# Kernel tuning notes

Hardware: AMD Instinct MI355X
Metric: run time of the kernel (lower is better)

Reference implementation:

```python
import jax, jax.numpy as jnp
import numpy as np

LAYERS, STACKS = 10, 4
DILATIONS = [2 ** l for _ in range(STACKS) for l in range(LAYERS)]  # 40 blocks


def setup_inputs() -> dict:
    key = jax.random.key(0)
    ks = jax.random.split(key, 7)
    B, C, L, SC, NB = 4, 64, 8192, 256, len(DILATIONS)
    scale = 0.05  # keep 40 stacked residual blocks numerically tame
    return {
        "x": jax.random.normal(ks[0], (B, C, L), dtype=jnp.float32),
        "dc_w": jax.random.normal(ks[1], (NB, C, C, 2), dtype=jnp.float32) * scale,
        "dc_b": jax.random.normal(ks[2], (NB, C), dtype=jnp.float32) * scale,
        "conv_w": jax.random.normal(ks[3], (NB, C, C), dtype=jnp.float32) * scale,
        "conv_b": jax.random.normal(ks[4], (NB, C), dtype=jnp.float32) * scale,
        "skip_w": jax.random.normal(ks[5], (NB, SC, C), dtype=jnp.float32) * scale,
        "skip_b": jax.random.normal(ks[6], (NB, SC), dtype=jnp.float32) * scale,
        "skip_size": 4096,
    }


def reference(x, dc_w, dc_b, conv_w, conv_b, skip_w, skip_b, skip_size):
    # x: [B, res_ch, L]; returns stacked skips [n_blocks, B, skip_ch, skip_size]
    out = x
    skips = []
    for i, d in enumerate(DILATIONS):
        h = (jnp.einsum('oi,bil->bol', dc_w[i, :, :, 0], out[:, :, :-d])
             + jnp.einsum('oi,bil->bol', dc_w[i, :, :, 1], out[:, :, d:])
             + dc_b[i][None, :, None])
        g = jax.nn.relu(h)
        r = jnp.einsum('oi,bil->bol', conv_w[i], g) + conv_b[i][None, :, None]
        out = r + out[:, :, -r.shape[2]:]  # residual on aligned (last) timesteps
        s = jnp.einsum('oi,bil->bol', skip_w[i], g) + skip_b[i][None, :, None]
        skips.append(s[:, :, -skip_size:])
    return jnp.stack(skips)
```

## Files before the change

### kernel.cpp

```cpp
#include <hip/hip_runtime.h>


#define CC    64
#define SCC   256
#define BB    4
#define LL0   8192
#define NBLK  40
#define SKIPN 4096

typedef __attribute__((ext_vector_type(8))) short bf16x8;
typedef __attribute__((ext_vector_type(4))) float f32x4;
typedef unsigned short us;

__device__ __forceinline__ us f2bf(float f) {
    union { float f; unsigned u; } v; v.f = f;
    return (us)((v.u + 0x7FFF + ((v.u >> 16) & 1)) >> 16);
}
__device__ __forceinline__ unsigned pk2(float a, float b) {
    return (unsigned)f2bf(a) | ((unsigned)f2bf(b) << 16);
}
__device__ __forceinline__ uint2 pk4(f32x4 v) {
    return (uint2){pk2(v[0], v[1]), pk2(v[2], v[3])};
}
__device__ __forceinline__ bf16x8 pack8(f32x4 u0, f32x4 u1) {
    bf16x8 r;
    r[0]=(short)f2bf(u0[0]); r[1]=(short)f2bf(u0[1]);
    r[2]=(short)f2bf(u0[2]); r[3]=(short)f2bf(u0[3]);
    r[4]=(short)f2bf(u1[0]); r[5]=(short)f2bf(u1[1]);
    r[6]=(short)f2bf(u1[2]); r[7]=(short)f2bf(u1[3]);
    return r;
}
__device__ __forceinline__ int sws(int r, int c) {
    return (r << 6) + ((((c >> 3) ^ r) & 7) << 3) + (c & 7);
}
__device__ __forceinline__ int scb(int s, int chunk) {
    return (s << 6) + (((chunk ^ (s & 7)) & 7) << 3);
}

__global__ __launch_bounds__(256) void prep_kernel(
    const float* __restrict__ x, float* __restrict__ xt_out,
    const float* __restrict__ dc_w, const float* __restrict__ conv_w,
    const float* __restrict__ skip_w,
    us* __restrict__ wcat, us* __restrict__ cwb, us* __restrict__ swb)
{
    if (blockIdx.x < 512) {
        __shared__ float tile[64][65];
        const int b = blockIdx.x >> 7, t0 = (blockIdx.x & 127) * 64;
        const int tid = threadIdx.x;
        #pragma unroll
        for (int p = 0; p < 4; ++p) {
            const int c = p * 16 + (tid >> 4), j = tid & 15;
            const float4 v = *(const float4*)(x + ((size_t)b * CC + c) * LL0 + t0 + j * 4);
            tile[c][j*4+0]=v.x; tile[c][j*4+1]=v.y; tile[c][j*4+2]=v.z; tile[c][j*4+3]=v.w;
        }
        __syncthreads();
        #pragma unroll
        for (int p = 0; p < 4; ++p) {
            const int r = p * 16 + (tid >> 4), h = tid & 15;
            float4 v = {tile[h*4+0][r], tile[h*4+1][r], tile[h*4+2][r], tile[h*4+3][r]};
            *(float4*)(xt_out + ((size_t)b * LL0 + t0 + r) * CC + h * 4) = v;
        }
        return;
    }
    const int n_sw = NBLK * SCC * CC, n_cw = NBLK * CC * CC, n_wc = NBLK * CC * 128;
    for (int idx = (blockIdx.x - 512) * blockDim.x + threadIdx.x; idx < n_sw;
         idx += 1024 * blockDim.x) {
        swb[idx] = f2bf(skip_w[idx]);
        if (idx < n_cw) cwb[idx] = f2bf(conv_w[idx]);
        if (idx < n_wc) {
            const int i = idx >> 13, o = (idx >> 7) & 63, kk = idx & 127;
            wcat[idx] = f2bf(dc_w[(((i * CC + o) * CC) + (kk & 63)) * 2 + (kk >> 6)]);
        }
    }
}

template<int NW>
__device__ __forceinline__ void skip_body(
    int e, int blk0,
    const us* __restrict__ g_all, const us* __restrict__ swb,
    const float* __restrict__ skip_b, float* __restrict__ out)
{
    constexpr int ROWS = NW * 16;
    constexpr int TPB = (SKIPN / ROWS) * BB;
    const int tid = threadIdx.x, lane = tid & 63, wv = tid >> 6;
    const int j = blk0 + e / TPB;
    const int id = e % TPB;
    const int tt = id % (SKIPN / ROWS);
    const int b  = id / (SKIPN / ROWS);
    const us* g  = g_all + ((size_t)j * BB + b) * SKIPN * CC;
    const us* sw = swb + (size_t)j * SCC * CC;
    const float* sb = skip_b + j * SCC;
    float* op = out + ((size_t)j * BB + b) * SCC * SKIPN;

    const int trow = tt * ROWS + wv * 16 + (lane & 15);
    bf16x8 a[2];
    a[0] = *(const bf16x8*)(g + (size_t)trow * CC + (lane >> 4) * 8);
    a[1] = *(const bf16x8*)(g + (size_t)trow * CC + 32 + (lane >> 4) * 8);
    const int tstore = tt * ROWS + wv * 16 + ((lane >> 4) << 2);
    #pragma unroll 4
    for (int n = 0; n < 16; ++n) {
        const int sc = n * 16 + (lane & 15);
        const float bias = sb[sc];
        f32x4 acc = (f32x4){bias, bias, bias, bias};
        const us* wrow = sw + sc * CC + (lane >> 4) * 8;
        acc = __builtin_amdgcn_mfma_f32_16x16x32_bf16(a[0], *(const bf16x8*)(wrow), acc, 0, 0, 0);
        acc = __builtin_amdgcn_mfma_f32_16x16x32_bf16(a[1], *(const bf16x8*)(wrow + 32), acc, 0, 0, 0);
        *(float4*)(op + (size_t)sc * SKIPN + tstore) = (float4){acc[0], acc[1], acc[2], acc[3]};
    }
}

__global__ __launch_bounds__(512) void fused6_kernel(
    const float* __restrict__ cur, float* __restrict__ nxt,
    const us* __restrict__ wcat_all, const us* __restrict__ cwb_all,
    const float* __restrict__ db_all, const float* __restrict__ cb_all,
    us* __restrict__ g_all, int blk0, int Lin, int ntiles,
    const us* __restrict__ swb, const float* __restrict__ skip_b,
    float* __restrict__ out, int pb0)
{
    const int wg = blockIdx.x, chain = BB * ntiles;
    if (wg >= chain) { skip_body<8>(wg - chain, pb0, g_all, swb, skip_b, out); return; }

    constexpr int TOUT = 96, R0 = 159, RCAP = 160;
    __shared__ __align__(16) float sm[RCAP * CC];
    __shared__ __align__(16) us  scr[8 * 16 * CC];

    const int tid = threadIdx.x, lane = tid & 63, wv = tid >> 6;
    const int b = wg / ntiles, t0 = (wg % ntiles) * TOUT;
    const float* src = cur + (size_t)b * LL0 * CC;
    const int s = lane & 15, q = lane >> 4;
    us* myscr = scr + wv * (16 * CC);

    for (int base = 0; base < R0; base += 32) {
        const int row = base + (tid >> 4);
        const int h4 = (tid & 15) * 4;
        if (row < R0) {
            int gt = t0 + row; if (gt > Lin - 1) gt = Lin - 1;
            *(f32x4*)(sm + sws(row, h4)) = *(const f32x4*)(src + (size_t)gt * CC + h4);
        }
    }
    __syncthreads();

    int Rcur = R0, Lj = Lin;
    for (int j = 0; j < 6; ++j) {
        const int d = 1 << j;
        const int Rn = Rcur - d;
        Lj -= d;
        const us* wj = wcat_all + (size_t)(blk0 + j) * CC * 128;
        const us* cj = cwb_all + (size_t)(blk0 + j) * CC * CC;
        const float* dbj = db_all + (blk0 + j) * CC;
        const float* cbj = cb_all + (blk0 + j) * CC;
        const int wbase = Lj - SKIPN;
        us* gdst = g_all + ((size_t)(blk0 + j) * BB + b) * SKIPN * CC;

        f32x4 r2[2][4];
        #pragma unroll
        for (int fi = 0; fi < 2; ++fi) {
            const int fg = wv + fi * 8;
            const bool act = fg * 16 < Rn;
            if (act) {
                const int t = fg * 16 + s;
                const int tc = t > Rn - 1 ? Rn - 1 : t;
                bf16x8 af0 = pack8(*(const f32x4*)(sm + sws(tc, q * 8)),
                                   *(const f32x4*)(sm + sws(tc, q * 8 + 4)));
                bf16x8 af1 = pack8(*(const f32x4*)(sm + sws(tc, 32 + q * 8)),
                                   *(const f32x4*)(sm + sws(tc, 36 + q * 8)));
                bf16x8 af2 = pack8(*(const f32x4*)(sm + sws(tc + d, q * 8)),
                                   *(const f32x4*)(sm + sws(tc + d, q * 8 + 4)));
                bf16x8 af3 = pack8(*(const f32x4*)(sm + sws(tc + d, 32 + q * 8)),
                                   *(const f32x4*)(sm + sws(tc + d, 36 + q * 8)));
                #pragma unroll
                for (int n = 0; n < 4; ++n) {
                    const int o0 = n * 16 + q * 4;
                    f32x4 acc = *(const f32x4*)(dbj + o0);
                    const us* wr = wj + (n * 16 + s) * 128 + q * 8;
                    acc = __builtin_amdgcn_mfma_f32_16x16x32_bf16(*(const bf16x8*)(wr),      af0, acc, 0, 0, 0);
                    acc = __builtin_amdgcn_mfma_f32_16x16x32_bf16(*(const bf16x8*)(wr + 32), af1, acc, 0, 0, 0);
                    acc = __builtin_amdgcn_mfma_f32_16x16x32_bf16(*(const bf16x8*)(wr + 64), af2, acc, 0, 0, 0);
                    acc = __builtin_amdgcn_mfma_f32_16x16x32_bf16(*(const bf16x8*)(wr + 96), af3, acc, 0, 0, 0);
                    #pragma unroll
                    for (int r = 0; r < 4; ++r) acc[r] = acc[r] > 0.f ? acc[r] : 0.f;
                    *(uint2*)(myscr + scb(s, n * 2 + (q >> 1)) + (q & 1) * 4) = pk4(acc);
                }
                {
                    const int gt = t0 + t;
                    if (t < Rn && gt >= wbase && gt < Lj) {
                        us* gr = gdst + (size_t)(gt - wbase) * CC;
                        #pragma unroll
                        for (int h = 0; h < 2; ++h) {
                            const int ck = q * 2 + h;
                            *(bf16x8*)(gr + ck * 8) = *(const bf16x8*)(myscr + scb(s, ck));
                        }
                    }
                }
                bf16x8 g0 = *(const bf16x8*)(myscr + scb(s, q));
                bf16x8 g1 = *(const bf16x8*)(myscr + scb(s, 4 + q));
                #pragma unroll
                for (int n = 0; n < 4; ++n) {
                    const int o0 = n * 16 + q * 4;
                    f32x4 r = *(const f32x4*)(cbj + o0);
                    const us* wr = cj + (n * 16 + s) * CC + q * 8;
                    r = __builtin_amdgcn_mfma_f32_16x16x32_bf16(*(const bf16x8*)(wr),      g0, r, 0, 0, 0);
                    r = __builtin_amdgcn_mfma_f32_16x16x32_bf16(*(const bf16x8*)(wr + 32), g1, r, 0, 0, 0);
                    r += *(const f32x4*)(sm + sws(tc + d, o0));
                    r2[fi][n] = r;
                }
            }
        }
        __syncthreads();
        #pragma unroll
        for (int fi = 0; fi < 2; ++fi) {
            const int fg = wv + fi * 8;
            const int t = fg * 16 + s;
            if (t < Rn) {
                #pragma unroll
                for (int n = 0; n < 4; ++n)
                    *(f32x4*)(sm + sws(t, n * 16 + q * 4)) = r2[fi][n];
            }
        }
        __syncthreads();
        Rcur = Rn;
    }

    float* dst = nxt + (size_t)b * LL0 * CC;
    for (int base = 0; base < TOUT; base += 32) {
        const int row = base + (tid >> 4);
        const int h4 = (tid & 15) * 4;
        const int gt = t0 + row;
        if (row < TOUT && gt < Lj)
            *(float4*)(dst + (size_t)gt * CC + h4) = *(const float4*)(sm + sws(row, h4));
    }
}

template<int D>
__global__ __launch_bounds__(256) void pair_kernel(
    const float* __restrict__ cur, float* __restrict__ nxt,
    const us* __restrict__ wA, const us* __restrict__ wB,
    const us* __restrict__ cA, const us* __restrict__ cB,
    const float* __restrict__ dbA, const float* __restrict__ dbB,
    const float* __restrict__ cbA, const float* __restrict__ cbB,
    us* __restrict__ gA_out, us* __restrict__ gB_out,
    int Lin, int ntB,
    const us* __restrict__ g_all, const us* __restrict__ swb,
    const float* __restrict__ skip_b, float* __restrict__ out, int pb0)
{
    const int wg = blockIdx.x, chain = BB * ntB;
    if (wg >= chain) { skip_body<4>(wg - chain, pb0, g_all, swb, skip_b, out); return; }

    __shared__ __align__(16) float xs[4 * 32 * CC];
    __shared__ __align__(16) float ms[2 * 32 * CC];
    __shared__ __align__(16) us  scr[4 * 16 * CC];

    const int tid = threadIdx.x, lane = tid & 63, wv = tid >> 6;
    const int b = wg / ntB, T0 = (wg % ntB) * 32;
    const float* src = cur + (size_t)b * LL0 * CC;
    const int s = lane & 15, q = lane >> 4;
    us* myscr = scr + wv * (16 * CC);
    const int LoutA = Lin - D, Lout2 = Lin - 3 * D;

    #pragma unroll
    for (int p = 0; p < 8; ++p) {
        const int row = p * 16 + (tid >> 4);
        const int st = row >> 5, r = row & 31;
        const int h4 = (tid & 15) * 4;
        int gt = T0 + st * D + r; if (gt > Lin - 1) gt = Lin - 1;
        *(f32x4*)(xs + st * (32 * CC) + sws(r, h4)) =
            *(const f32x4*)(src + (size_t)gt * CC + h4);
    }
    __syncthreads();

    {
        const int m = wv >> 1, rA = (wv & 1) * 16 + s;
        const int tA = T0 + m * 2 * D + rA;
        const float* x0 = xs + (2 * m) * (32 * CC);
        const float* x1 = xs + (2 * m + 1) * (32 * CC);
        bf16x8 af0 = pack8(*(const f32x4*)(x0 + sws(rA, q * 8)),
                           *(const f32x4*)(x0 + sws(rA, q * 8 + 4)));
        bf16x8 af1 = pack8(*(const f32x4*)(x0 + sws(rA, 32 + q * 8)),
                           *(const f32x4*)(x0 + sws(rA, 36 + q * 8)));
        bf16x8 af2 = pack8(*(const f32x4*)(x1 + sws(rA, q * 8)),
                           *(const f32x4*)(x1 + sws(rA, q * 8 + 4)));
        bf16x8 af3 = pack8(*(const f32x4*)(x1 + sws(rA, 32 + q * 8)),
                           *(const f32x4*)(x1 + sws(rA, 36 + q * 8)));
        #pragma unroll
        for (int n = 0; n < 4; ++n) {
            const int o0 = n * 16 + q * 4;
            f32x4 acc = *(const f32x4*)(dbA + o0);
            const us* wr = wA + (n * 16 + s) * 128 + q * 8;
            acc = __builtin_amdgcn_mfma_f32_16x16x32_bf16(*(const bf16x8*)(wr),      af0, acc, 0, 0, 0);
            acc = __builtin_amdgcn_mfma_f32_16x16x32_bf16(*(const bf16x8*)(wr + 32), af1, acc, 0, 0, 0);
            acc = __builtin_amdgcn_mfma_f32_16x16x32_bf16(*(const bf16x8*)(wr + 64), af2, acc, 0, 0, 0);
            acc = __builtin_amdgcn_mfma_f32_16x16x32_bf16(*(const bf16x8*)(wr + 96), af3, acc, 0, 0, 0);
            #pragma unroll
            for (int r = 0; r < 4; ++r) acc[r] = acc[r] > 0.f ? acc[r] : 0.f;
            *(uint2*)(myscr + scb(s, n * 2 + (q >> 1)) + (q & 1) * 4) = pk4(acc);
        }
        {
            const int wbA = LoutA - SKIPN;
            const bool own = (m == 0) || (tA >= ntB * 32);
            if (own && tA >= wbA && tA < LoutA) {
                us* gr = gA_out + ((size_t)b * SKIPN + (tA - wbA)) * CC;
                #pragma unroll
                for (int h = 0; h < 2; ++h) {
                    const int ck = q * 2 + h;
                    *(bf16x8*)(gr + ck * 8) = *(const bf16x8*)(myscr + scb(s, ck));
                }
            }
        }
        bf16x8 g0 = *(const bf16x8*)(myscr + scb(s, q));
        bf16x8 g1 = *(const bf16x8*)(myscr + scb(s, 4 + q));
        #pragma unroll
        for (int n = 0; n < 4; ++n) {
            const int o0 = n * 16 + q * 4;
            f32x4 r = *(const f32x4*)(cbA + o0);
            const us* wr = cA + (n * 16 + s) * CC + q * 8;
            r = __builtin_amdgcn_mfma_f32_16x16x32_bf16(*(const bf16x8*)(wr),      g0, r, 0, 0, 0);
            r = __builtin_amdgcn_mfma_f32_16x16x32_bf16(*(const bf16x8*)(wr + 32), g1, r, 0, 0, 0);
            r += *(const f32x4*)(x1 + sws(rA, o0));
            *(f32x4*)(ms + m * (32 * CC) + sws(rA, o0)) = r;
        }
    }
    __syncthreads();

    {
        const int rB = (wv & 1) * 16 + s;
        const int tB = T0 + rB;
        const bool lead = wv < 2;
        const float* m0 = ms;
        const float* m1 = ms + 32 * CC;
        bf16x8 af0 = pack8(*(const f32x4*)(m0 + sws(rB, q * 8)),
                           *(const f32x4*)(m0 + sws(rB, q * 8 + 4)));
        bf16x8 af1 = pack8(*(const f32x4*)(m0 + sws(rB, 32 + q * 8)),
                           *(const f32x4*)(m0 + sws(rB, 36 + q * 8)));
        bf16x8 af2 = pack8(*(const f32x4*)(m1 + sws(rB, q * 8)),
                           *(const f32x4*)(m1 + sws(rB, q * 8 + 4)));
        bf16x8 af3 = pack8(*(const f32x4*)(m1 + sws(rB, 32 + q * 8)),
                           *(const f32x4*)(m1 + sws(rB, 36 + q * 8)));
        #pragma unroll
        for (int n = 0; n < 4; ++n) {
            const int o0 = n * 16 + q * 4;
            f32x4 acc = *(const f32x4*)(dbB + o0);
            const us* wr = wB + (n * 16 + s) * 128 + q * 8;
            acc = __builtin_amdgcn_mfma_f32_16x16x32_bf16(*(const bf16x8*)(wr),      af0, acc, 0, 0, 0);
            acc = __builtin_amdgcn_mfma_f32_16x16x32_bf16(*(const bf16x8*)(wr + 32), af1, acc, 0, 0, 0);
            acc = __builtin_amdgcn_mfma_f32_16x16x32_bf16(*(const bf16x8*)(wr + 64), af2, acc, 0, 0, 0);
            acc = __builtin_amdgcn_mfma_f32_16x16x32_bf16(*(const bf16x8*)(wr + 96), af3, acc, 0, 0, 0);
            #pragma unroll
            for (int r = 0; r < 4; ++r) acc[r] = acc[r] > 0.f ? acc[r] : 0.f;
            *(uint2*)(myscr + scb(s, n * 2 + (q >> 1)) + (q & 1) * 4) = pk4(acc);
        }
        {
            const int wbB = Lout2 - SKIPN;
            if (lead && tB >= wbB && tB < Lout2) {
                us* gr = gB_out + ((size_t)b * SKIPN + (tB - wbB)) * CC;
                #pragma unroll
                for (int h = 0; h < 2; ++h) {
                    const int ck = q * 2 + h;
                    *(bf16x8*)(gr + ck * 8) = *(const bf16x8*)(myscr + scb(s, ck));
                }
            }
        }
        bf16x8 g0 = *(const bf16x8*)(myscr + scb(s, q));
        bf16x8 g1 = *(const bf16x8*)(myscr + scb(s, 4 + q));
        float* dst = nxt + (size_t)b * LL0 * CC;
        #pragma unroll
        for (int n = 0; n < 4; ++n) {
            const int o0 = n * 16 + q * 4;
            f32x4 r = *(const f32x4*)(cbB + o0);
            const us* wr = cB + (n * 16 + s) * CC + q * 8;
            r = __builtin_amdgcn_mfma_f32_16x16x32_bf16(*(const bf16x8*)(wr),      g0, r, 0, 0, 0);
            r = __builtin_amdgcn_mfma_f32_16x16x32_bf16(*(const bf16x8*)(wr + 32), g1, r, 0, 0, 0);
            r += *(const f32x4*)(m1 + sws(rB, o0));
            if (lead && tB < Lout2)
                *(f32x4*)(dst + (size_t)tB * CC + o0) = r;
        }
    }
}

__global__ __launch_bounds__(256) void skip_kernel(
    const us* __restrict__ g_all, const us* __restrict__ swb,
    const float* __restrict__ skip_b, float* __restrict__ out, int blk0)
{
    skip_body<4>(blockIdx.x, blk0, g_all, swb, skip_b, out);
}

extern "C" void kernel_launch(void* const* d_in, const int* in_sizes, int n_in,
                              void* d_out, int out_size, void* d_ws, size_t ws_size,
                              hipStream_t stream)
{
    const float* x      = (const float*)d_in[0];
    const float* dc_w   = (const float*)d_in[1];
    const float* dc_b   = (const float*)d_in[2];
    const float* conv_w = (const float*)d_in[3];
    const float* conv_b = (const float*)d_in[4];
    const float* skip_w = (const float*)d_in[5];
    const float* skip_b = (const float*)d_in[6];
    float* out = (float*)d_out;

    char* ws = (char*)d_ws;
    float* bufA = (float*)ws;  ws += (size_t)BB * LL0 * CC * 4;
    float* bufB = (float*)ws;  ws += (size_t)BB * LL0 * CC * 4;
    us* g_all = (us*)ws;       ws += (size_t)NBLK * BB * SKIPN * CC * 2;
    us* wcat  = (us*)ws;       ws += (size_t)NBLK * CC * 128 * 2;
    us* cwb   = (us*)ws;       ws += (size_t)NBLK * CC * CC * 2;
    us* swb   = (us*)ws;       ws += (size_t)NBLK * SCC * CC * 2;

    prep_kernel<<<1536, 256, 0, stream>>>(x, bufA, dc_w, conv_w, skip_w, wcat, cwb, swb);

    float* bufs[2] = {bufA, bufB};
    const size_t GSZ = (size_t)BB * SKIPN * CC;
    int Lc = LL0, blk = 0, q = 0, produced = 0, skipped = 0;
    for (int st = 0; st < 4; ++st) {
        {
            const int Lout = Lc - 63;
            const int nt = (Lout + 95) / 96;
            int cap = produced - skipped; if (cap > 4) cap = 4;
            fused6_kernel<<<dim3(BB * nt + cap * 128), 512, 0, stream>>>(
                bufs[q & 1], bufs[(q + 1) & 1], wcat, cwb, dc_b, conv_b,
                g_all, blk, Lc, nt, swb, skip_b, out, skipped);
            skipped += cap; produced += 6; blk += 6; Lc = Lout; ++q;
        }
        #pragma unroll
        for (int pi = 0; pi < 2; ++pi) {
            const int D = pi == 0 ? 64 : 256;
            const int Lout2 = Lc - 3 * D;
            const int nt = (Lout2 + 31) / 32;
            int cap = produced - skipped; if (cap > 4) cap = 4;
            const int grid = BB * nt + cap * 256;
            if (D == 64)
                pair_kernel<64><<<dim3(grid), 256, 0, stream>>>(
                    bufs[q & 1], bufs[(q + 1) & 1],
                    wcat + (size_t)blk * CC * 128, wcat + (size_t)(blk + 1) * CC * 128,
                    cwb + (size_t)blk * CC * CC, cwb + (size_t)(blk + 1) * CC * CC,
                    dc_b + blk * CC, dc_b + (blk + 1) * CC,
                    conv_b + blk * CC, conv_b + (blk + 1) * CC,
                    g_all + (size_t)blk * GSZ, g_all + (size_t)(blk + 1) * GSZ,
                    Lc, nt, g_all, swb, skip_b, out, skipped);
            else
                pair_kernel<256><<<dim3(grid), 256, 0, stream>>>(
                    bufs[q & 1], bufs[(q + 1) & 1],
                    wcat + (size_t)blk * CC * 128, wcat + (size_t)(blk + 1) * CC * 128,
                    cwb + (size_t)blk * CC * CC, cwb + (size_t)(blk + 1) * CC * CC,
                    dc_b + blk * CC, dc_b + (blk + 1) * CC,
                    conv_b + blk * CC, conv_b + (blk + 1) * CC,
                    g_all + (size_t)blk * GSZ, g_all + (size_t)(blk + 1) * GSZ,
                    Lc, nt, g_all, swb, skip_b, out, skipped);
            skipped += cap; produced += 2; blk += 2; Lc = Lout2; ++q;
        }
    }
    const int rem = NBLK - skipped;
    if (rem > 0)
        skip_kernel<<<dim3(rem * 256), 256, 0, stream>>>(g_all, swb, skip_b, out, skipped);
}
```

Baseline: 770.5 us.

## Fuse skip projection into residual chain kernels and keep bf16 activation copies in LDS

```diff
diff --git a/kernel.cpp b/kernel.cpp
--- a/kernel.cpp
+++ b/kernel.cpp
@@ -22,15 +22,10 @@
 __device__ __forceinline__ uint2 pk4(f32x4 v) {
     return (uint2){pk2(v[0], v[1]), pk2(v[2], v[3])};
 }
-__device__ __forceinline__ bf16x8 pack8(f32x4 u0, f32x4 u1) {
-    bf16x8 r;
-    r[0]=(short)f2bf(u0[0]); r[1]=(short)f2bf(u0[1]);
-    r[2]=(short)f2bf(u0[2]); r[3]=(short)f2bf(u0[3]);
-    r[4]=(short)f2bf(u1[0]); r[5]=(short)f2bf(u1[1]);
-    r[6]=(short)f2bf(u1[2]); r[7]=(short)f2bf(u1[3]);
-    return r;
-}
 __device__ __forceinline__ int sws(int r, int c) {
+    return (r << 6) + ((((c >> 3) ^ r) & 7) << 3) + (c & 7);
+}
+__device__ __forceinline__ int swh(int r, int c) {
     return (r << 6) + ((((c >> 3) ^ r) & 7) << 3) + (c & 7);
 }
 __device__ __forceinline__ int scb(int s, int chunk) {
@@ -74,38 +69,32 @@
     }
 }
 
-template<int NW>
-__device__ __forceinline__ void skip_body(
-    int e, int blk0,
-    const us* __restrict__ g_all, const us* __restrict__ swb,
-    const float* __restrict__ skip_b, float* __restrict__ out)
-{
-    constexpr int ROWS = NW * 16;
-    constexpr int TPB = (SKIPN / ROWS) * BB;
-    const int tid = threadIdx.x, lane = tid & 63, wv = tid >> 6;
-    const int j = blk0 + e / TPB;
-    const int id = e % TPB;
-    const int tt = id % (SKIPN / ROWS);
-    const int b  = id / (SKIPN / ROWS);
-    const us* g  = g_all + ((size_t)j * BB + b) * SKIPN * CC;
-    const us* sw = swb + (size_t)j * SCC * CC;
-    const float* sb = skip_b + j * SCC;
-    float* op = out + ((size_t)j * BB + b) * SCC * SKIPN;
-
-    const int trow = tt * ROWS + wv * 16 + (lane & 15);
-    bf16x8 a[2];
-    a[0] = *(const bf16x8*)(g + (size_t)trow * CC + (lane >> 4) * 8);
-    a[1] = *(const bf16x8*)(g + (size_t)trow * CC + 32 + (lane >> 4) * 8);
-    const int tstore = tt * ROWS + wv * 16 + ((lane >> 4) << 2);
+__device__ __forceinline__ void skip16(
+    bf16x8 g0, bf16x8 g1,
+    const us* __restrict__ sw, const float* __restrict__ sb,
+    float* __restrict__ op, int tbase, int wb, int Lend,
+    int s, int q, int nlo, int nhi)
+{
+    if (tbase + 15 < wb || tbase >= Lend) return;
+    const int t4 = tbase + q * 4;
+    const bool fullvec = (t4 >= wb) && (t4 + 3 < Lend);
     #pragma unroll 4
-    for (int n = 0; n < 16; ++n) {
-        const int sc = n * 16 + (lane & 15);
+    for (int n = nlo; n < nhi; ++n) {
+        const int sc = n * 16 + s;
         const float bias = sb[sc];
         f32x4 acc = (f32x4){bias, bias, bias, bias};
-        const us* wrow = sw + sc * CC + (lane >> 4) * 8;
-        acc = __builtin_amdgcn_mfma_f32_16x16x32_bf16(a[0], *(const bf16x8*)(wrow), acc, 0, 0, 0);
-        acc = __builtin_amdgcn_mfma_f32_16x16x32_bf16(a[1], *(const bf16x8*)(wrow + 32), acc, 0, 0, 0);
-        *(float4*)(op + (size_t)sc * SKIPN + tstore) = (float4){acc[0], acc[1], acc[2], acc[3]};
+        const us* wr = sw + sc * CC + q * 8;
+        acc = __builtin_amdgcn_mfma_f32_16x16x32_bf16(g0, *(const bf16x8*)(wr),      acc, 0, 0, 0);
+        acc = __builtin_amdgcn_mfma_f32_16x16x32_bf16(g1, *(const bf16x8*)(wr + 32), acc, 0, 0, 0);
+        if (fullvec) {
+            *(float4*)(op + (size_t)sc * SKIPN + (t4 - wb)) =
+                (float4){acc[0], acc[1], acc[2], acc[3]};
+        } else {
+            #pragma unroll
+            for (int r = 0; r < 4; ++r)
+                if (t4 + r >= wb && t4 + r < Lend)
+                    op[(size_t)sc * SKIPN + (t4 + r - wb)] = acc[r];
+        }
     }
 }
 
@@ -113,19 +102,18 @@
     const float* __restrict__ cur, float* __restrict__ nxt,
     const us* __restrict__ wcat_all, const us* __restrict__ cwb_all,
     const float* __restrict__ db_all, const float* __restrict__ cb_all,
-    us* __restrict__ g_all, int blk0, int Lin, int ntiles,
-    const us* __restrict__ swb, const float* __restrict__ skip_b,
-    float* __restrict__ out, int pb0)
-{
-    const int wg = blockIdx.x, chain = BB * ntiles;
-    if (wg >= chain) { skip_body<8>(wg - chain, pb0, g_all, swb, skip_b, out); return; }
-
+    const us* __restrict__ swb_all, const float* __restrict__ sb_all,
+    float* __restrict__ out_all, int blk0, int Lin, int ntiles)
+{
     constexpr int TOUT = 96, R0 = 159, RCAP = 160;
     __shared__ __align__(16) float sm[RCAP * CC];
+    __shared__ __align__(16) us  smb[RCAP * CC];
     __shared__ __align__(16) us  scr[8 * 16 * CC];
 
     const int tid = threadIdx.x, lane = tid & 63, wv = tid >> 6;
-    const int b = wg / ntiles, t0 = (wg % ntiles) * TOUT;
+    const int b = blockIdx.x / ntiles, tix = blockIdx.x % ntiles;
+    const int t0 = tix * TOUT;
+    const bool lastt = (tix == ntiles - 1);
     const float* src = cur + (size_t)b * LL0 * CC;
     const int s = lane & 15, q = lane >> 4;
     us* myscr = scr + wv * (16 * CC);
@@ -135,7 +123,9 @@
         const int h4 = (tid & 15) * 4;
         if (row < R0) {
             int gt = t0 + row; if (gt > Lin - 1) gt = Lin - 1;
-            *(f32x4*)(sm + sws(row, h4)) = *(const f32x4*)(src + (size_t)gt * CC + h4);
+            f32x4 v = *(const f32x4*)(src + (size_t)gt * CC + h4);
+            *(f32x4*)(sm + sws(row, h4)) = v;
+            *(uint2*)(smb + swh(row, h4)) = pk4(v);
         }
     }
     __syncthreads();
@@ -147,27 +137,23 @@
         Lj -= d;
         const us* wj = wcat_all + (size_t)(blk0 + j) * CC * 128;
         const us* cj = cwb_all + (size_t)(blk0 + j) * CC * CC;
+        const us* sj = swb_all + (size_t)(blk0 + j) * SCC * CC;
         const float* dbj = db_all + (blk0 + j) * CC;
         const float* cbj = cb_all + (blk0 + j) * CC;
-        const int wbase = Lj - SKIPN;
-        us* gdst = g_all + ((size_t)(blk0 + j) * BB + b) * SKIPN * CC;
+        const float* sbj = sb_all + (blk0 + j) * SCC;
+        float* opj = out_all + ((size_t)(blk0 + j) * BB + b) * SCC * SKIPN;
 
         f32x4 r2[2][4];
         #pragma unroll
         for (int fi = 0; fi < 2; ++fi) {
             const int fg = wv + fi * 8;
-            const bool act = fg * 16 < Rn;
-            if (act) {
+            if (fg * 16 < Rn) {
                 const int t = fg * 16 + s;
                 const int tc = t > Rn - 1 ? Rn - 1 : t;
-                bf16x8 af0 = pack8(*(const f32x4*)(sm + sws(tc, q * 8)),
-                                   *(const f32x4*)(sm + sws(tc, q * 8 + 4)));
-                bf16x8 af1 = pack8(*(const f32x4*)(sm + sws(tc, 32 + q * 8)),
-                                   *(const f32x4*)(sm + sws(tc, 36 + q * 8)));
-                bf16x8 af2 = pack8(*(const f32x4*)(sm + sws(tc + d, q * 8)),
-                                   *(const f32x4*)(sm + sws(tc + d, q * 8 + 4)));
-                bf16x8 af3 = pack8(*(const f32x4*)(sm + sws(tc + d, 32 + q * 8)),
-                                   *(const f32x4*)(sm + sws(tc + d, 36 + q * 8)));
+                bf16x8 af0 = *(const bf16x8*)(smb + swh(tc,     q * 8));
+                bf16x8 af1 = *(const bf16x8*)(smb + swh(tc,     32 + q * 8));
+                bf16x8 af2 = *(const bf16x8*)(smb + swh(tc + d, q * 8));
+                bf16x8 af3 = *(const bf16x8*)(smb + swh(tc + d, 32 + q * 8));
                 #pragma unroll
                 for (int n = 0; n < 4; ++n) {
                     const int o0 = n * 16 + q * 4;
@@ -181,17 +167,6 @@
                     for (int r = 0; r < 4; ++r) acc[r] = acc[r] > 0.f ? acc[r] : 0.f;
                     *(uint2*)(myscr + scb(s, n * 2 + (q >> 1)) + (q & 1) * 4) = pk4(acc);
                 }
-                {
-                    const int gt = t0 + t;
-                    if (t < Rn && gt >= wbase && gt < Lj) {
-                        us* gr = gdst + (size_t)(gt - wbase) * CC;
-                        #pragma unroll
-                        for (int h = 0; h < 2; ++h) {
-                            const int ck = q * 2 + h;
-                            *(bf16x8*)(gr + ck * 8) = *(const bf16x8*)(myscr + scb(s, ck));
-                        }
-                    }
-                }
                 bf16x8 g0 = *(const bf16x8*)(myscr + scb(s, q));
                 bf16x8 g1 = *(const bf16x8*)(myscr + scb(s, 4 + q));
                 #pragma unroll
@@ -204,6 +179,10 @@
                     r += *(const f32x4*)(sm + sws(tc + d, o0));
                     r2[fi][n] = r;
                 }
+                const bool own96 = (fi == 0 && wv < 6);
+                if (own96 || lastt)
+                    skip16(g0, g1, sj, sbj, opj, t0 + fg * 16,
+                           Lj - SKIPN, Lj, s, q, 0, 16);
             }
         }
         __syncthreads();
@@ -213,8 +192,11 @@
             const int t = fg * 16 + s;
             if (t < Rn) {
                 #pragma unroll
-                for (int n = 0; n < 4; ++n)
-                    *(f32x4*)(sm + sws(t, n * 16 + q * 4)) = r2[fi][n];
+                for (int n = 0; n < 4; ++n) {
+                    const int o0 = n * 16 + q * 4;
+                    *(f32x4*)(sm + sws(t, o0)) = r2[fi][n];
+                    *(uint2*)(smb + swh(t, o0)) = pk4(r2[fi][n]);
+                }
             }
         }
         __syncthreads();
@@ -238,20 +220,19 @@
     const us* __restrict__ cA, const us* __restrict__ cB,
     const float* __restrict__ dbA, const float* __restrict__ dbB,
     const float* __restrict__ cbA, const float* __restrict__ cbB,
-    us* __restrict__ gA_out, us* __restrict__ gB_out,
-    int Lin, int ntB,
-    const us* __restrict__ g_all, const us* __restrict__ swb,
-    const float* __restrict__ skip_b, float* __restrict__ out, int pb0)
-{
-    const int wg = blockIdx.x, chain = BB * ntB;
-    if (wg >= chain) { skip_body<4>(wg - chain, pb0, g_all, swb, skip_b, out); return; }
-
-    __shared__ __align__(16) float xs[4 * 32 * CC];
-    __shared__ __align__(16) float ms[2 * 32 * CC];
-    __shared__ __align__(16) us  scr[4 * 16 * CC];
+    const us* __restrict__ swA, const us* __restrict__ swB,
+    const float* __restrict__ sbA, const float* __restrict__ sbB,
+    float* __restrict__ outA, float* __restrict__ outB,
+    int Lin, int ntB)
+{
+    __shared__ __align__(16) us   xsb[4 * 32 * CC];
+    __shared__ __align__(16) float xf[2 * 32 * CC];
+    __shared__ __align__(16) us   msb[2 * 32 * CC];
+    __shared__ __align__(16) float mf[32 * CC];
+    __shared__ __align__(16) us   scr[4 * 16 * CC];
 
     const int tid = threadIdx.x, lane = tid & 63, wv = tid >> 6;
-    const int b = wg / ntB, T0 = (wg % ntB) * 32;
+    const int b = blockIdx.x / ntB, T0 = (blockIdx.x % ntB) * 32;
     const float* src = cur + (size_t)b * LL0 * CC;
     const int s = lane & 15, q = lane >> 4;
     us* myscr = scr + wv * (16 * CC);
@@ -263,24 +244,22 @@
         const int st = row >> 5, r = row & 31;
         const int h4 = (tid & 15) * 4;
         int gt = T0 + st * D + r; if (gt > Lin - 1) gt = Lin - 1;
-        *(f32x4*)(xs + st * (32 * CC) + sws(r, h4)) =
-            *(const f32x4*)(src + (size_t)gt * CC + h4);
+        f32x4 v = *(const f32x4*)(src + (size_t)gt * CC + h4);
+        *(uint2*)(xsb + st * (32 * CC) + swh(r, h4)) = pk4(v);
+        if (st & 1) *(f32x4*)(xf + (st >> 1) * (32 * CC) + sws(r, h4)) = v;
     }
     __syncthreads();
 
     {
         const int m = wv >> 1, rA = (wv & 1) * 16 + s;
-        const int tA = T0 + m * 2 * D + rA;
-        const float* x0 = xs + (2 * m) * (32 * CC);
-        const float* x1 = xs + (2 * m + 1) * (32 * CC);
-        bf16x8 af0 = pack8(*(const f32x4*)(x0 + sws(rA, q * 8)),
-                           *(const f32x4*)(x0 + sws(rA, q * 8 + 4)));
-        bf16x8 af1 = pack8(*(const f32x4*)(x0 + sws(rA, 32 + q * 8)),
-                           *(const f32x4*)(x0 + sws(rA, 36 + q * 8)));
-        bf16x8 af2 = pack8(*(const f32x4*)(x1 + sws(rA, q * 8)),
-                           *(const f32x4*)(x1 + sws(rA, q * 8 + 4)));
-        bf16x8 af3 = pack8(*(const f32x4*)(x1 + sws(rA, 32 + q * 8)),
-                           *(const f32x4*)(x1 + sws(rA, 36 + q * 8)));
+        const int tgrp = T0 + m * 2 * D + (wv & 1) * 16;
+        const us* x0b = xsb + (2 * m) * (32 * CC);
+        const us* x1b = xsb + (2 * m + 1) * (32 * CC);
+        const float* x1f = xf + m * (32 * CC);
+        bf16x8 af0 = *(const bf16x8*)(x0b + swh(rA, q * 8));
+        bf16x8 af1 = *(const bf16x8*)(x0b + swh(rA, 32 + q * 8));
+        bf16x8 af2 = *(const bf16x8*)(x1b + swh(rA, q * 8));
+        bf16x8 af3 = *(const bf16x8*)(x1b + swh(rA, 32 + q * 8));
         #pragma unroll
         for (int n = 0; n < 4; ++n) {
             const int o0 = n * 16 + q * 4;
@@ -294,20 +273,11 @@
             for (int r = 0; r < 4; ++r) acc[r] = acc[r] > 0.f ? acc[r] : 0.f;
             *(uint2*)(myscr + scb(s, n * 2 + (q >> 1)) + (q & 1) * 4) = pk4(acc);
         }
-        {
-            const int wbA = LoutA - SKIPN;
-            const bool own = (m == 0) || (tA >= ntB * 32);
-            if (own && tA >= wbA && tA < LoutA) {
-                us* gr = gA_out + ((size_t)b * SKIPN + (tA - wbA)) * CC;
-                #pragma unroll
-                for (int h = 0; h < 2; ++h) {
-                    const int ck = q * 2 + h;
-                    *(bf16x8*)(gr + ck * 8) = *(const bf16x8*)(myscr + scb(s, ck));
-                }
-            }
-        }
         bf16x8 g0 = *(const bf16x8*)(myscr + scb(s, q));
         bf16x8 g1 = *(const bf16x8*)(myscr + scb(s, 4 + q));
+        if (m == 0 || tgrp >= ntB * 32)
+            skip16(g0, g1, swA, sbA, outA + (size_t)b * SCC * SKIPN,
+                   tgrp, LoutA - SKIPN, LoutA, s, q, 0, 16);
         #pragma unroll
         for (int n = 0; n < 4; ++n) {
             const int o0 = n * 16 + q * 4;
@@ -315,8 +285,9 @@
             const us* wr = cA + (n * 16 + s) * CC + q * 8;
             r = __builtin_amdgcn_mfma_f32_16x16x32_bf16(*(const bf16x8*)(wr),      g0, r, 0, 0, 0);
             r = __builtin_amdgcn_mfma_f32_16x16x32_bf16(*(const bf16x8*)(wr + 32), g1, r, 0, 0, 0);
-            r += *(const f32x4*)(x1 + sws(rA, o0));
-            *(f32x4*)(ms + m * (32 * CC) + sws(rA, o0)) = r;
+            r += *(const f32x4*)(x1f + sws(rA, o0));
+            *(uint2*)(msb + m * (32 * CC) + swh(rA, o0)) = pk4(r);
+            if (m == 1) *(f32x4*)(mf + sws(rA, o0)) = r;
         }
     }
     __syncthreads();
@@ -324,17 +295,12 @@
     {
         const int rB = (wv & 1) * 16 + s;
         const int tB = T0 + rB;
+        const int tgrp = T0 + (wv & 1) * 16;
         const bool lead = wv < 2;
-        const float* m0 = ms;
-        const float* m1 = ms + 32 * CC;
-        bf16x8 af0 = pack8(*(const f32x4*)(m0 + sws(rB, q * 8)),
-                           *(const f32x4*)(m0 + sws(rB, q * 8 + 4)));
-        bf16x8 af1 = pack8(*(const f32x4*)(m0 + sws(rB, 32 + q * 8)),
-                           *(const f32x4*)(m0 + sws(rB, 36 + q * 8)));
-        bf16x8 af2 = pack8(*(const f32x4*)(m1 + sws(rB, q * 8)),
-                           *(const f32x4*)(m1 + sws(rB, q * 8 + 4)));
-        bf16x8 af3 = pack8(*(const f32x4*)(m1 + sws(rB, 32 + q * 8)),
-                           *(const f32x4*)(m1 + sws(rB, 36 + q * 8)));
+        bf16x8 af0 = *(const bf16x8*)(msb + swh(rB, q * 8));
+        bf16x8 af1 = *(const bf16x8*)(msb + swh(rB, 32 + q * 8));
+        bf16x8 af2 = *(const bf16x8*)(msb + (32 * CC) + swh(rB, q * 8));
+        bf16x8 af3 = *(const bf16x8*)(msb + (32 * CC) + swh(rB, 32 + q * 8));
         #pragma unroll
         for (int n = 0; n < 4; ++n) {
             const int o0 = n * 16 + q * 4;
@@ -348,19 +314,10 @@
             for (int r = 0; r < 4; ++r) acc[r] = acc[r] > 0.f ? acc[r] : 0.f;
             *(uint2*)(myscr + scb(s, n * 2 + (q >> 1)) + (q & 1) * 4) = pk4(acc);
         }
-        {
-            const int wbB = Lout2 - SKIPN;
-            if (lead && tB >= wbB && tB < Lout2) {
-                us* gr = gB_out + ((size_t)b * SKIPN + (tB - wbB)) * CC;
-                #pragma unroll
-                for (int h = 0; h < 2; ++h) {
-                    const int ck = q * 2 + h;
-                    *(bf16x8*)(gr + ck * 8) = *(const bf16x8*)(myscr + scb(s, ck));
-                }
-            }
-        }
         bf16x8 g0 = *(const bf16x8*)(myscr + scb(s, q));
         bf16x8 g1 = *(const bf16x8*)(myscr + scb(s, 4 + q));
+        skip16(g0, g1, swB, sbB, outB + (size_t)b * SCC * SKIPN,
+               tgrp, Lout2 - SKIPN, Lout2, s, q, lead ? 0 : 8, lead ? 8 : 16);
         float* dst = nxt + (size_t)b * LL0 * CC;
         #pragma unroll
         for (int n = 0; n < 4; ++n) {
@@ -369,18 +326,11 @@
             const us* wr = cB + (n * 16 + s) * CC + q * 8;
             r = __builtin_amdgcn_mfma_f32_16x16x32_bf16(*(const bf16x8*)(wr),      g0, r, 0, 0, 0);
             r = __builtin_amdgcn_mfma_f32_16x16x32_bf16(*(const bf16x8*)(wr + 32), g1, r, 0, 0, 0);
-            r += *(const f32x4*)(m1 + sws(rB, o0));
+            r += *(const f32x4*)(mf + sws(rB, o0));
             if (lead && tB < Lout2)
                 *(f32x4*)(dst + (size_t)tB * CC + o0) = r;
         }
     }
-}
-
-__global__ __launch_bounds__(256) void skip_kernel(
-    const us* __restrict__ g_all, const us* __restrict__ swb,
-    const float* __restrict__ skip_b, float* __restrict__ out, int blk0)
-{
-    skip_body<4>(blockIdx.x, blk0, g_all, swb, skip_b, out);
 }
 
 extern "C" void kernel_launch(void* const* d_in, const int* in_sizes, int n_in,
@@ -399,55 +349,51 @@
     char* ws = (char*)d_ws;
     float* bufA = (float*)ws;  ws += (size_t)BB * LL0 * CC * 4;
     float* bufB = (float*)ws;  ws += (size_t)BB * LL0 * CC * 4;
-    us* g_all = (us*)ws;       ws += (size_t)NBLK * BB * SKIPN * CC * 2;
-    us* wcat  = (us*)ws;       ws += (size_t)NBLK * CC * 128 * 2;
-    us* cwb   = (us*)ws;       ws += (size_t)NBLK * CC * CC * 2;
-    us* swb   = (us*)ws;       ws += (size_t)NBLK * SCC * CC * 2;
+    us* wcat = (us*)ws;        ws += (size_t)NBLK * CC * 128 * 2;
+    us* cwb  = (us*)ws;        ws += (size_t)NBLK * CC * CC * 2;
+    us* swb  = (us*)ws;        ws += (size_t)NBLK * SCC * CC * 2;
 
     prep_kernel<<<1536, 256, 0, stream>>>(x, bufA, dc_w, conv_w, skip_w, wcat, cwb, swb);
 
     float* bufs[2] = {bufA, bufB};
-    const size_t GSZ = (size_t)BB * SKIPN * CC;
-    int Lc = LL0, blk = 0, q = 0, produced = 0, skipped = 0;
+    const size_t OSZ = (size_t)BB * SCC * SKIPN;
+    int Lc = LL0, blk = 0, qq = 0;
     for (int st = 0; st < 4; ++st) {
         {
             const int Lout = Lc - 63;
             const int nt = (Lout + 95) / 96;
-            int cap = produced - skipped; if (cap > 4) cap = 4;
-            fused6_kernel<<<dim3(BB * nt + cap * 128), 512, 0, stream>>>(
-                bufs[q & 1], bufs[(q + 1) & 1], wcat, cwb, dc_b, conv_b,
-                g_all, blk, Lc, nt, swb, skip_b, out, skipped);
-            skipped += cap; produced += 6; blk += 6; Lc = Lout; ++q;
-        }
-        #pragma unroll
+            fused6_kernel<<<dim3(BB * nt), 512, 0, stream>>>(
+                bufs[qq & 1], bufs[(qq + 1) & 1], wcat, cwb, dc_b, conv_b,
+                swb, skip_b, out, blk, Lc, nt);
+            blk += 6; Lc = Lout; ++qq;
+        }
         for (int pi = 0; pi < 2; ++pi) {
             const int D = pi == 0 ? 64 : 256;
             const int Lout2 = Lc - 3 * D;
             const int nt = (Lout2 + 31) / 32;
-            int cap = produced - skipped; if (cap > 4) cap = 4;
-            const int grid = BB * nt + cap * 256;
             if (D == 64)
-                pair_kernel<64><<<dim3(grid), 256, 0, stream>>>(
-                    bufs[q & 1], bufs[(q + 1) & 1],
+                pair_kernel<64><<<dim3(BB * nt), 256, 0, stream>>>(
+                    bufs[qq & 1], bufs[(qq + 1) & 1],
                     wcat + (size_t)blk * CC * 128, wcat + (size_t)(blk + 1) * CC * 128,
                     cwb + (size_t)blk * CC * CC, cwb + (size_t)(blk + 1) * CC * CC,
                     dc_b + blk * CC, dc_b + (blk + 1) * CC,
                     conv_b + blk * CC, conv_b + (blk + 1) * CC,
-                    g_all + (size_t)blk * GSZ, g_all + (size_t)(blk + 1) * GSZ,
-                    Lc, nt, g_all, swb, skip_b, out, skipped);
+                    swb + (size_t)blk * SCC * CC, swb + (size_t)(blk + 1) * SCC * CC,
+                    skip_b + blk * SCC, skip_b + (blk + 1) * SCC,
+                    out + (size_t)blk * OSZ, out + (size_t)(blk + 1) * OSZ,
+                    Lc, nt);
             else
-                pair_kernel<256><<<dim3(grid), 256, 0, stream>>>(
-                    bufs[q & 1], bufs[(q + 1) & 1],
+                pair_kernel<256><<<dim3(BB * nt), 256, 0, stream>>>(
+                    bufs[qq & 1], bufs[(qq + 1) & 1],
                     wcat + (size_t)blk * CC * 128, wcat + (size_t)(blk + 1) * CC * 128,
                     cwb + (size_t)blk * CC * CC, cwb + (size_t)(blk + 1) * CC * CC,
                     dc_b + blk * CC, dc_b + (blk + 1) * CC,
                     conv_b + blk * CC, conv_b + (blk + 1) * CC,
-                    g_all + (size_t)blk * GSZ, g_all + (size_t)(blk + 1) * GSZ,
-                    Lc, nt, g_all, swb, skip_b, out, skipped);
-            skipped += cap; produced += 2; blk += 2; Lc = Lout2; ++q;
-        }
-    }
-    const int rem = NBLK - skipped;
-    if (rem > 0)
-        skip_kernel<<<dim3(rem * 256), 256, 0, stream>>>(g_all, swb, skip_b, out, skipped);
-}
+                    swb + (size_t)blk * SCC * CC, swb + (size_t)(blk + 1) * SCC * CC,
+                    skip_b + blk * SCC, skip_b + (blk + 1) * SCC,
+                    out + (size_t)blk * OSZ, out + (size_t)(blk + 1) * OSZ,
+                    Lc, nt);
+            blk += 2; Lc = Lout2; ++qq;
+        }
+    }
+}
```

Result: slower. 1.015 ms (+31.8%).
